# Performance work log

Measured on AMD Instinct MI355X. Metric: run time of the kernel, lower is better.

## Reference

```python
import jax, jax.numpy as jnp
import numpy as np

HIDDEN = 1024
HEADS = 16
HEAD_D = HIDDEN // HEADS
B = 64
MAX_S = 2048
EPS = 1e-5


def _layernorm(x, gamma, beta):
    mu = jnp.mean(x, axis=-1, keepdims=True)
    var = jnp.mean(jnp.square(x - mu), axis=-1, keepdims=True)
    return (x - mu) * jax.lax.rsqrt(var + EPS) * gamma + beta


def setup_inputs() -> dict:
    key = jax.random.key(0)
    ks = jax.random.split(key, 12)
    s = 1.0 / np.sqrt(HIDDEN)
    return {
        "seq": jax.random.normal(ks[0], (B, 1, HIDDEN), jnp.float32),
        "candidate_aa": jax.random.normal(ks[1], (B, 1, HIDDEN), jnp.float32),
        "k_cache": jax.random.normal(ks[2], (B, MAX_S, HEADS, HEAD_D), jnp.float32),
        "v_cache": jax.random.normal(ks[3], (B, MAX_S, HEADS, HEAD_D), jnp.float32),
        "cache_seqlens": jax.random.randint(ks[4], (B,), 0, MAX_S - 1, jnp.int32),
        "Wqkv": jax.random.normal(ks[5], (HIDDEN, 3 * HIDDEN), jnp.float32) * s,
        "bqkv": jnp.zeros((3 * HIDDEN,), jnp.float32),
        "Wc": jax.random.normal(ks[6], (HIDDEN, HIDDEN), jnp.float32) * s,
        "bc": jnp.zeros((HIDDEN,), jnp.float32),
        "Wo": jax.random.normal(ks[7], (HIDDEN, HIDDEN), jnp.float32) * s,
        "bo": jnp.zeros((HIDDEN,), jnp.float32),
        "gamma": jnp.ones((HIDDEN,), jnp.float32),
        "beta": jnp.zeros((HIDDEN,), jnp.float32),
    }


def reference(seq, candidate_aa, k_cache, v_cache, cache_seqlens,
              Wqkv, bqkv, Wc, bc, Wo, bo, gamma, beta):
    b = seq.shape[0]
    # fused QKV projection: [B,1,3*hidden] -> [B,1,H,3*D] -> chunk
    qkv = (seq @ Wqkv + bqkv).reshape(b, 1, HEADS, 3 * HEAD_D)
    q, k, v = jnp.split(qkv, 3, axis=-1)  # each [B,1,H,D]
    cand = candidate_aa @ Wc + bc
    # L2-normalize new k along head dim, then fp16 cast (as original)
    k = k / jnp.linalg.norm(k, axis=-1, keepdims=True)
    k = k.astype(jnp.float16).astype(k_cache.dtype)
    # write new token into caches at position cache_seqlens[b]
    bidx = jnp.arange(b)
    kc = k_cache.at[bidx, cache_seqlens].set(k[:, 0])
    vc = v_cache.at[bidx, cache_seqlens].set(v[:, 0])
    # attention over cache[:, :seqlen+1], softmax_scale = 1
    scores = jnp.einsum("bhd,bshd->bhs", q[:, 0], kc)  # [B,H,S]
    valid = jnp.arange(MAX_S)[None, None, :] <= cache_seqlens[:, None, None]
    scores = jnp.where(valid, scores, jnp.finfo(scores.dtype).min)
    p = jax.nn.softmax(scores, axis=-1)
    attn = jnp.einsum("bhs,bshd->bhd", p, vc).reshape(b, 1, HIDDEN)
    postx = attn @ Wo + bo
    candidate_out = _layernorm(postx + cand, gamma, beta)
    seq_out = _layernorm(seq + postx, gamma, beta)
    return (seq_out, candidate_out)
```

## Files before the change

### kernel.cpp

```cpp
#include <hip/hip_runtime.h>
#include <hip/hip_fp16.h>
#include <math.h>

#define HID   1024
#define NHEAD 16
#define HD    64
#define NB    64
#define MAXS  2048
#define CHUNK 256
#define NCH   (MAXS / CHUNK)
#define PS    68

typedef float f4v __attribute__((ext_vector_type(4)));
__device__ __forceinline__ float4 ntload4(const float* p) {
    f4v v = __builtin_nontemporal_load((const f4v*)p);
    return make_float4(v.x, v.y, v.z, v.w);
}

__global__ __launch_bounds__(1024) void proj_kernel(
    const float* __restrict__ seq, const float* __restrict__ cand,
    const float* __restrict__ Wqkv, const float* __restrict__ bqkv,
    const float* __restrict__ Wc,   const float* __restrict__ bcv,
    float* __restrict__ out )
{
    const int tid  = threadIdx.x;
    const int wv   = __builtin_amdgcn_readfirstlane(tid >> 6);
    const int lane = tid & 63;
    const int c0   = blockIdx.x * 16;
    const bool is_qkv = (c0 < 3072);
    const float* __restrict__ src  = is_qkv ? seq  : cand;
    const float* __restrict__ W    = is_qkv ? Wqkv : Wc;
    const float* __restrict__ bias = is_qkv ? bqkv : bcv;
    const int ldw = is_qkv ? 3072 : 1024;
    const int cb  = is_qkv ? c0 : (c0 - 3072);
    const int k0  = wv * 64;

    float acc[16];
    #pragma unroll
    for (int j = 0; j < 16; ++j) acc[j] = 0.f;

    const float4* sp = (const float4*)(src + lane * HID + k0);
    for (int kc = 0; kc < 16; ++kc) {
        float4 s4 = sp[kc];
        const float* wb = W + (size_t)(k0 + kc * 4) * ldw + cb;
        #pragma unroll
        for (int t = 0; t < 4; ++t) {
            float sv = (t == 0) ? s4.x : (t == 1) ? s4.y : (t == 2) ? s4.z : s4.w;
            const float4* wr = (const float4*)(wb + (size_t)t * ldw);
            #pragma unroll
            for (int j = 0; j < 4; ++j) {
                float4 w4 = wr[j];
                acc[4*j+0] = fmaf(sv, w4.x, acc[4*j+0]);
                acc[4*j+1] = fmaf(sv, w4.y, acc[4*j+1]);
                acc[4*j+2] = fmaf(sv, w4.z, acc[4*j+2]);
                acc[4*j+3] = fmaf(sv, w4.w, acc[4*j+3]);
            }
        }
    }

    __shared__ float red[16][16][64];
    #pragma unroll
    for (int j = 0; j < 16; ++j) red[wv][j][lane] = acc[j];
    __syncthreads();

    {
        const int j = tid >> 6, b = tid & 63;
        float s = 0.f;
        #pragma unroll
        for (int w = 0; w < 16; ++w) s += red[w][j][b];
        out[(c0 + j) * 64 + b] = s + bias[cb + j];
    }
}

__global__ __launch_bounds__(256) void attn_part_kernel(
    const float* __restrict__ proj, const float* __restrict__ k_cache,
    const float* __restrict__ v_cache, const int* __restrict__ seqlens,
    float* __restrict__ part)
{
    const int idx = blockIdx.x;
    const int c  = idx >> 10;
    const int bh = idx & 1023;
    const int b  = bh >> 4;
    const int h  = bh & 15;
    const int L  = seqlens[b];
    const int s0 = c << 8;
    if (s0 > L) return;

    const int tid = threadIdx.x;
    const int grp = tid >> 4;
    const int gl  = tid & 15;
    const bool has_new = (L < s0 + CHUNK);

    __shared__ float lq[64], lk[64], lv[64];
    __shared__ float sm_m[16], sm_l[16];
    __shared__ float sm_o[16][64];

    if (tid < 64) {
        lq[tid] = proj[(h * 192 + tid) * 64 + b];
    } else if (tid < 128) {
        if (has_new) {
            int d = tid - 64;
            float kr = proj[(h * 192 + 64 + d) * 64 + b];
            float ss = kr * kr;
            #pragma unroll
            for (int m = 1; m < 64; m <<= 1) ss += __shfl_xor(ss, m);
            float kn = kr / sqrtf(ss);
            lk[d] = __half2float(__float2half_rn(kn));
        }
    } else if (tid < 192) {
        if (has_new) {
            int d = tid - 128;
            lv[d] = proj[(h * 192 + 128 + d) * 64 + b];
        }
    }
    __syncthreads();

    const float4 q4 = ((const float4*)lq)[gl];
    const size_t base0 = (((size_t)b * MAXS) * NHEAD + h) * HD;

    float sc[16];
    float m, l;
    float4 o = make_float4(0.f, 0.f, 0.f, 0.f);

    if (!has_new) {
        #pragma unroll
        for (int t = 0; t < 16; ++t) {
            const int s = s0 + grp + t * 16;
            float4 k4 = ntload4(k_cache + base0 + (size_t)s * (NHEAD * HD) + gl * 4);
            float d = fmaf(k4.x, q4.x, fmaf(k4.y, q4.y, fmaf(k4.z, q4.z, k4.w * q4.w)));
            d += __shfl_xor(d, 1); d += __shfl_xor(d, 2);
            d += __shfl_xor(d, 4); d += __shfl_xor(d, 8);
            sc[t] = d;
        }
        m = sc[0];
        #pragma unroll
        for (int t = 1; t < 16; ++t) m = fmaxf(m, sc[t]);
        l = 0.f;
        #pragma unroll
        for (int t = 0; t < 16; ++t) { float p = __expf(sc[t] - m); sc[t] = p; l += p; }
        #pragma unroll
        for (int t = 0; t < 16; ++t) {
            const int s = s0 + grp + t * 16;
            float4 v4 = ntload4(v_cache + base0 + (size_t)s * (NHEAD * HD) + gl * 4);
            o.x = fmaf(sc[t], v4.x, o.x);
            o.y = fmaf(sc[t], v4.y, o.y);
            o.z = fmaf(sc[t], v4.z, o.z);
            o.w = fmaf(sc[t], v4.w, o.w);
        }
    } else {
        #pragma unroll
        for (int t = 0; t < 16; ++t) {
            const int s = s0 + grp + t * 16;
            float4 k4 = make_float4(0.f, 0.f, 0.f, 0.f);
            if (s < L)       k4 = ntload4(k_cache + base0 + (size_t)s * (NHEAD * HD) + gl * 4);
            else if (s == L) k4 = ((const float4*)lk)[gl];
            float d = fmaf(k4.x, q4.x, fmaf(k4.y, q4.y, fmaf(k4.z, q4.z, k4.w * q4.w)));
            d += __shfl_xor(d, 1); d += __shfl_xor(d, 2);
            d += __shfl_xor(d, 4); d += __shfl_xor(d, 8);
            sc[t] = (s <= L) ? d : -INFINITY;
        }
        m = sc[0];
        #pragma unroll
        for (int t = 1; t < 16; ++t) m = fmaxf(m, sc[t]);
        const float mm = (m == -INFINITY) ? 0.f : m;
        l = 0.f;
        #pragma unroll
        for (int t = 0; t < 16; ++t) { float p = __expf(sc[t] - mm); sc[t] = p; l += p; }
        #pragma unroll
        for (int t = 0; t < 16; ++t) {
            const int s = s0 + grp + t * 16;
            float4 v4 = make_float4(0.f, 0.f, 0.f, 0.f);
            if (s < L)       v4 = ntload4(v_cache + base0 + (size_t)s * (NHEAD * HD) + gl * 4);
            else if (s == L) v4 = ((const float4*)lv)[gl];
            o.x = fmaf(sc[t], v4.x, o.x);
            o.y = fmaf(sc[t], v4.y, o.y);
            o.z = fmaf(sc[t], v4.z, o.z);
            o.w = fmaf(sc[t], v4.w, o.w);
        }
    }

    if (gl == 0) { sm_m[grp] = m; sm_l[grp] = l; }
    ((float4*)sm_o[grp])[gl] = o;
    __syncthreads();

    if (tid < 64) {
        float M = -INFINITY;
        #pragma unroll
        for (int g = 0; g < 16; ++g) M = fmaxf(M, sm_m[g]);
        float li = 0.f, oi = 0.f;
        #pragma unroll
        for (int g = 0; g < 16; ++g) {
            float w = __expf(sm_m[g] - M);
            li += w * sm_l[g];
            oi += w * sm_o[g][tid];
        }
        float* pb = part + (size_t)(c * 1024 + bh) * PS;
        pb[tid] = oi;
        if (tid == 0) { pb[64] = M; pb[65] = li; }
    }
}

__global__ __launch_bounds__(64) void attn_merge_kernel(
    const float* __restrict__ part, const int* __restrict__ seqlens,
    float* __restrict__ attn_out )
{
    const int bh = blockIdx.x;
    const int b  = bh >> 4;
    const int h  = bh & 15;
    const int d  = threadIdx.x;
    const int nch = (seqlens[b] >> 8) + 1;

    float M = -INFINITY, l = 0.f, o = 0.f;
    for (int c = 0; c < nch; ++c) {
        const float* pb = part + (size_t)(c * 1024 + bh) * PS;
        float mc = pb[64], lc = pb[65];
        float Mn = fmaxf(M, mc);
        float f = __expf(M - Mn);
        float w = __expf(mc - Mn);
        o = o * f + w * pb[d];
        l = l * f + w * lc;
        M = Mn;
    }
    attn_out[(h * 64 + d) * 64 + b] = o / l;
}

__global__ __launch_bounds__(1024) void wo_kernel(
    const float* __restrict__ attn_s, const float* __restrict__ Wo,
    const float* __restrict__ bo, float* __restrict__ postx )
{
    const int tid  = threadIdx.x;
    const int wv   = __builtin_amdgcn_readfirstlane(tid >> 6);
    const int lane = tid & 63;
    const int c0   = blockIdx.x * 8;
    const int k0   = wv * 64;

    float acc[8];
    #pragma unroll
    for (int j = 0; j < 8; ++j) acc[j] = 0.f;

    for (int k = 0; k < 64; ++k) {
        float sv = attn_s[(k0 + k) * 64 + lane];
        const float4* wr = (const float4*)(Wo + (size_t)(k0 + k) * 1024 + c0);
        float4 w0 = wr[0], w1 = wr[1];
        acc[0] = fmaf(sv, w0.x, acc[0]); acc[1] = fmaf(sv, w0.y, acc[1]);
        acc[2] = fmaf(sv, w0.z, acc[2]); acc[3] = fmaf(sv, w0.w, acc[3]);
        acc[4] = fmaf(sv, w1.x, acc[4]); acc[5] = fmaf(sv, w1.y, acc[5]);
        acc[6] = fmaf(sv, w1.z, acc[6]); acc[7] = fmaf(sv, w1.w, acc[7]);
    }

    __shared__ float red[16][8][64];
    #pragma unroll
    for (int j = 0; j < 8; ++j) red[wv][j][lane] = acc[j];
    __syncthreads();

    if (tid < 512) {
        const int j = tid >> 6, b = tid & 63;
        float s = 0.f;
        #pragma unroll
        for (int w = 0; w < 16; ++w) s += red[w][j][b];
        postx[(c0 + j) * 64 + b] = s + bo[c0 + j];
    }
}

__global__ __launch_bounds__(256) void ln_kernel(
    const float* __restrict__ seq, const float* __restrict__ cand_s,
    const float* __restrict__ postx, const float* __restrict__ gamma,
    const float* __restrict__ beta, float* __restrict__ out)
{
    const int b   = blockIdx.x;
    const int tid = threadIdx.x;
    float x1[4], x2[4];
    float s1 = 0.f, q1 = 0.f, s2 = 0.f, q2 = 0.f;

    #pragma unroll
    for (int i = 0; i < 4; ++i) {
        int c = tid + i * 256;
        float px = postx[c * 64 + b];
        float sv = seq[b * HID + c];
        float cd = cand_s[c * 64 + b];
        float a = sv + px, d = px + cd;
        x1[i] = a; x2[i] = d;
        s1 += a; q1 += a * a; s2 += d; q2 += d * d;
    }
    #pragma unroll
    for (int m = 1; m < 64; m <<= 1) {
        s1 += __shfl_xor(s1, m); q1 += __shfl_xor(q1, m);
        s2 += __shfl_xor(s2, m); q2 += __shfl_xor(q2, m);
    }
    __shared__ float rsm[4][4];
    const int wv = tid >> 6, lane = tid & 63;
    if (lane == 0) { rsm[wv][0] = s1; rsm[wv][1] = q1; rsm[wv][2] = s2; rsm[wv][3] = q2; }
    __syncthreads();

    float S1 = rsm[0][0] + rsm[1][0] + rsm[2][0] + rsm[3][0];
    float Q1 = rsm[0][1] + rsm[1][1] + rsm[2][1] + rsm[3][1];
    float S2 = rsm[0][2] + rsm[1][2] + rsm[2][2] + rsm[3][2];
    float Q2 = rsm[0][3] + rsm[1][3] + rsm[2][3] + rsm[3][3];

    const float inv = 1.f / 1024.f;
    float mu1 = S1 * inv, v1 = Q1 * inv - mu1 * mu1;
    float mu2 = S2 * inv, v2 = Q2 * inv - mu2 * mu2;
    float r1 = rsqrtf(v1 + 1e-5f);
    float r2 = rsqrtf(v2 + 1e-5f);

    #pragma unroll
    for (int i = 0; i < 4; ++i) {
        int c = tid + i * 256;
        float g = gamma[c], be = beta[c];
        out[b * HID + c]            = (x1[i] - mu1) * r1 * g + be;
        out[NB * HID + b * HID + c] = (x2[i] - mu2) * r2 * g + be;
    }
}

extern "C" void kernel_launch(void* const* d_in, const int* in_sizes, int n_in,
                              void* d_out, int out_size, void* d_ws, size_t ws_size,
                              hipStream_t stream) {
    const float* seq      = (const float*)d_in[0];
    const float* cand     = (const float*)d_in[1];
    const float* k_cache  = (const float*)d_in[2];
    const float* v_cache  = (const float*)d_in[3];
    const int*   seqlens  = (const int*)  d_in[4];
    const float* Wqkv     = (const float*)d_in[5];
    const float* bqkv     = (const float*)d_in[6];
    const float* Wc       = (const float*)d_in[7];
    const float* bcv      = (const float*)d_in[8];
    const float* Wo       = (const float*)d_in[9];
    const float* bo       = (const float*)d_in[10];
    const float* gamma    = (const float*)d_in[11];
    const float* beta     = (const float*)d_in[12];
    float* out = (float*)d_out;

    float* ws    = (float*)d_ws;
    float* proj  = ws;
    float* attn  = proj  + 4096 * 64;
    float* postx = attn  + 1024 * 64;
    float* part  = postx + 1024 * 64;

    proj_kernel      <<<256, 1024, 0, stream>>>(seq, cand, Wqkv, bqkv, Wc, bcv, proj);
    attn_part_kernel <<<NCH * 1024, 256, 0, stream>>>(proj, k_cache, v_cache, seqlens, part);
    attn_merge_kernel<<<NB * NHEAD, 64, 0, stream>>>(part, seqlens, attn);
    wo_kernel        <<<128, 1024, 0, stream>>>(attn, Wo, bo, postx);
    ln_kernel        <<<NB, 256, 0, stream>>>(seq, proj + 3072 * 64, postx, gamma, beta, out);
}
```

Baseline: 149.5 us.

## Fuse attention merge, Wo projection and layernorms into one per-batch kernel

Replaces the merge, Wo GEMV and layernorm kernels with a single kernel that runs one 1024-thread block per batch row. Each block merges the chunk partials into a shared-memory attention row, multiplies it by the full Wo matrix, and applies both layernorms. This removes two launches and the global round trips for attn and postx. In exchange each of the 64 blocks streams all of Wo (4 MB) separately instead of the GEMV sharing weight loads across the batch, and only 64 blocks occupy the GPU.

```diff
diff --git a/kernel.cpp b/kernel.cpp
--- a/kernel.cpp
+++ b/kernel.cpp
@@ -200,116 +200,88 @@
     }
 }
 
-__global__ __launch_bounds__(64) void attn_merge_kernel(
-    const float* __restrict__ part, const int* __restrict__ seqlens,
-    float* __restrict__ attn_out )
-{
-    const int bh = blockIdx.x;
-    const int b  = bh >> 4;
-    const int h  = bh & 15;
-    const int d  = threadIdx.x;
-    const int nch = (seqlens[b] >> 8) + 1;
-
-    float M = -INFINITY, l = 0.f, o = 0.f;
-    for (int c = 0; c < nch; ++c) {
-        const float* pb = part + (size_t)(c * 1024 + bh) * PS;
-        float mc = pb[64], lc = pb[65];
-        float Mn = fmaxf(M, mc);
-        float f = __expf(M - Mn);
-        float w = __expf(mc - Mn);
-        o = o * f + w * pb[d];
-        l = l * f + w * lc;
-        M = Mn;
-    }
-    attn_out[(h * 64 + d) * 64 + b] = o / l;
-}
-
-__global__ __launch_bounds__(1024) void wo_kernel(
-    const float* __restrict__ attn_s, const float* __restrict__ Wo,
-    const float* __restrict__ bo, float* __restrict__ postx )
-{
-    const int tid  = threadIdx.x;
-    const int wv   = __builtin_amdgcn_readfirstlane(tid >> 6);
-    const int lane = tid & 63;
-    const int c0   = blockIdx.x * 8;
-    const int k0   = wv * 64;
-
-    float acc[8];
-    #pragma unroll
-    for (int j = 0; j < 8; ++j) acc[j] = 0.f;
-
-    for (int k = 0; k < 64; ++k) {
-        float sv = attn_s[(k0 + k) * 64 + lane];
-        const float4* wr = (const float4*)(Wo + (size_t)(k0 + k) * 1024 + c0);
-        float4 w0 = wr[0], w1 = wr[1];
-        acc[0] = fmaf(sv, w0.x, acc[0]); acc[1] = fmaf(sv, w0.y, acc[1]);
-        acc[2] = fmaf(sv, w0.z, acc[2]); acc[3] = fmaf(sv, w0.w, acc[3]);
-        acc[4] = fmaf(sv, w1.x, acc[4]); acc[5] = fmaf(sv, w1.y, acc[5]);
-        acc[6] = fmaf(sv, w1.z, acc[6]); acc[7] = fmaf(sv, w1.w, acc[7]);
-    }
-
-    __shared__ float red[16][8][64];
-    #pragma unroll
-    for (int j = 0; j < 8; ++j) red[wv][j][lane] = acc[j];
-    __syncthreads();
-
-    if (tid < 512) {
-        const int j = tid >> 6, b = tid & 63;
-        float s = 0.f;
-        #pragma unroll
-        for (int w = 0; w < 16; ++w) s += red[w][j][b];
-        postx[(c0 + j) * 64 + b] = s + bo[c0 + j];
-    }
-}
-
-__global__ __launch_bounds__(256) void ln_kernel(
-    const float* __restrict__ seq, const float* __restrict__ cand_s,
-    const float* __restrict__ postx, const float* __restrict__ gamma,
-    const float* __restrict__ beta, float* __restrict__ out)
+__global__ __launch_bounds__(1024) void post_kernel(
+    const float* __restrict__ proj, const float* __restrict__ part,
+    const int* __restrict__ seqlens, const float* __restrict__ Wo,
+    const float* __restrict__ bo, const float* __restrict__ seq,
+    const float* __restrict__ gamma, const float* __restrict__ beta,
+    float* __restrict__ out)
 {
     const int b   = blockIdx.x;
     const int tid = threadIdx.x;
-    float x1[4], x2[4];
-    float s1 = 0.f, q1 = 0.f, s2 = 0.f, q2 = 0.f;
-
-    #pragma unroll
-    for (int i = 0; i < 4; ++i) {
-        int c = tid + i * 256;
-        float px = postx[c * 64 + b];
-        float sv = seq[b * HID + c];
-        float cd = cand_s[c * 64 + b];
-        float a = sv + px, d = px + cd;
-        x1[i] = a; x2[i] = d;
-        s1 += a; q1 += a * a; s2 += d; q2 += d * d;
-    }
+    const int nch = (seqlens[b] >> 8) + 1;
+
+    __shared__ float attn_row[1024];
+    __shared__ float red[4][4][256];
+    __shared__ float rsm[16][4];
+
+    {
+        const int h = tid >> 6, d = tid & 63;
+        float M = -INFINITY, l = 0.f, o = 0.f;
+        for (int c = 0; c < nch; ++c) {
+            const float* pb = part + (size_t)(c * 1024 + b * 16 + h) * PS;
+            float mc = pb[64], lc = pb[65];
+            float Mn = fmaxf(M, mc);
+            float f = __expf(M - Mn);
+            float w = __expf(mc - Mn);
+            o = o * f + w * pb[d];
+            l = l * f + w * lc;
+            M = Mn;
+        }
+        attn_row[h * 64 + d] = o / l;
+    }
+    __syncthreads();
+
+    {
+        const int cg = tid & 255;
+        const int ks = tid >> 8;
+        float4 a = make_float4(0.f, 0.f, 0.f, 0.f);
+        const float* wp = Wo + (size_t)(ks * 256) * 1024 + cg * 4;
+        #pragma unroll 4
+        for (int k = 0; k < 256; ++k) {
+            float av = attn_row[ks * 256 + k];
+            float4 w4 = *(const float4*)(wp + (size_t)k * 1024);
+            a.x = fmaf(av, w4.x, a.x);
+            a.y = fmaf(av, w4.y, a.y);
+            a.z = fmaf(av, w4.z, a.z);
+            a.w = fmaf(av, w4.w, a.w);
+        }
+        red[ks][0][cg] = a.x; red[ks][1][cg] = a.y;
+        red[ks][2][cg] = a.z; red[ks][3][cg] = a.w;
+    }
+    __syncthreads();
+
+    const int c = tid;
+    float px = red[0][c & 3][c >> 2] + red[1][c & 3][c >> 2]
+             + red[2][c & 3][c >> 2] + red[3][c & 3][c >> 2] + bo[c];
+    float sv = seq[b * HID + c];
+    float cd = proj[(3072 + c) * 64 + b];
+    float x1 = sv + px, x2 = px + cd;
+
+    float s1 = x1, q1 = x1 * x1, s2 = x2, q2 = x2 * x2;
     #pragma unroll
     for (int m = 1; m < 64; m <<= 1) {
         s1 += __shfl_xor(s1, m); q1 += __shfl_xor(q1, m);
         s2 += __shfl_xor(s2, m); q2 += __shfl_xor(q2, m);
     }
-    __shared__ float rsm[4][4];
     const int wv = tid >> 6, lane = tid & 63;
     if (lane == 0) { rsm[wv][0] = s1; rsm[wv][1] = q1; rsm[wv][2] = s2; rsm[wv][3] = q2; }
     __syncthreads();
 
-    float S1 = rsm[0][0] + rsm[1][0] + rsm[2][0] + rsm[3][0];
-    float Q1 = rsm[0][1] + rsm[1][1] + rsm[2][1] + rsm[3][1];
-    float S2 = rsm[0][2] + rsm[1][2] + rsm[2][2] + rsm[3][2];
-    float Q2 = rsm[0][3] + rsm[1][3] + rsm[2][3] + rsm[3][3];
-
+    float S1 = 0.f, Q1 = 0.f, S2 = 0.f, Q2 = 0.f;
+    #pragma unroll
+    for (int w = 0; w < 16; ++w) {
+        S1 += rsm[w][0]; Q1 += rsm[w][1]; S2 += rsm[w][2]; Q2 += rsm[w][3];
+    }
     const float inv = 1.f / 1024.f;
     float mu1 = S1 * inv, v1 = Q1 * inv - mu1 * mu1;
     float mu2 = S2 * inv, v2 = Q2 * inv - mu2 * mu2;
     float r1 = rsqrtf(v1 + 1e-5f);
     float r2 = rsqrtf(v2 + 1e-5f);
 
-    #pragma unroll
-    for (int i = 0; i < 4; ++i) {
-        int c = tid + i * 256;
-        float g = gamma[c], be = beta[c];
-        out[b * HID + c]            = (x1[i] - mu1) * r1 * g + be;
-        out[NB * HID + b * HID + c] = (x2[i] - mu2) * r2 * g + be;
-    }
+    float g = gamma[c], be = beta[c];
+    out[b * HID + c]            = (x1 - mu1) * r1 * g + be;
+    out[NB * HID + b * HID + c] = (x2 - mu2) * r2 * g + be;
 }
 
 extern "C" void kernel_launch(void* const* d_in, const int* in_sizes, int n_in,
@@ -332,13 +304,9 @@
 
     float* ws    = (float*)d_ws;
     float* proj  = ws;
-    float* attn  = proj  + 4096 * 64;
-    float* postx = attn  + 1024 * 64;
-    float* part  = postx + 1024 * 64;
-
-    proj_kernel      <<<256, 1024, 0, stream>>>(seq, cand, Wqkv, bqkv, Wc, bcv, proj);
-    attn_part_kernel <<<NCH * 1024, 256, 0, stream>>>(proj, k_cache, v_cache, seqlens, part);
-    attn_merge_kernel<<<NB * NHEAD, 64, 0, stream>>>(part, seqlens, attn);
-    wo_kernel        <<<128, 1024, 0, stream>>>(attn, Wo, bo, postx);
-    ln_kernel        <<<NB, 256, 0, stream>>>(seq, proj + 3072 * 64, postx, gamma, beta, out);
-}
+    float* part  = proj + 4096 * 64;
+
+    proj_kernel     <<<256, 1024, 0, stream>>>(seq, cand, Wqkv, bqkv, Wc, bcv, proj);
+    attn_part_kernel<<<NCH * 1024, 256, 0, stream>>>(proj, k_cache, v_cache, seqlens, part);
+    post_kernel     <<<NB, 1024, 0, stream>>>(proj, part, seqlens, Wo, bo, seq, gamma, beta, out);
+}
```

New measurement: 165.4 us. +10.6%, slower.

## Split QKV/cand projection into split-K partial GEMV plus reduction kernel

Applied to the files above, without the earlier changes.

Replaces the single projection kernel with a split-K scheme. Each lane owns one output column and accumulates all 64 batch rows, reading each weight element once with nontemporal loads while the activations are broadcast from cache. A second kernel sums the 16 K-slice partials, adds the bias and writes a row-major projection buffer, and the attention and layernorm kernels now read that layout. This adds a kernel launch and a partial-sum buffer in global memory of about 16 MB written and read back, in exchange for better weight-stream efficiency.

```diff
diff --git a/kernel.cpp b/kernel.cpp
--- a/kernel.cpp
+++ b/kernel.cpp
@@ -10,70 +10,78 @@
 #define CHUNK 256
 #define NCH   (MAXS / CHUNK)
 #define PS    68
+#define NKS   16
 
 typedef float f4v __attribute__((ext_vector_type(4)));
 __device__ __forceinline__ float4 ntload4(const float* p) {
     f4v v = __builtin_nontemporal_load((const f4v*)p);
     return make_float4(v.x, v.y, v.z, v.w);
 }
-
-__global__ __launch_bounds__(1024) void proj_kernel(
+__device__ __forceinline__ float ntloadf(const float* p) {
+    return __builtin_nontemporal_load(p);
+}
+
+__global__ __launch_bounds__(256) void proj1_kernel(
     const float* __restrict__ seq, const float* __restrict__ cand,
-    const float* __restrict__ Wqkv, const float* __restrict__ bqkv,
-    const float* __restrict__ Wc,   const float* __restrict__ bcv,
-    float* __restrict__ out )
+    const float* __restrict__ Wqkv, const float* __restrict__ Wc,
+    float* __restrict__ partial )
 {
     const int tid  = threadIdx.x;
-    const int wv   = __builtin_amdgcn_readfirstlane(tid >> 6);
+    const int wv   = tid >> 6;
     const int lane = tid & 63;
-    const int c0   = blockIdx.x * 16;
-    const bool is_qkv = (c0 < 3072);
-    const float* __restrict__ src  = is_qkv ? seq  : cand;
-    const float* __restrict__ W    = is_qkv ? Wqkv : Wc;
-    const float* __restrict__ bias = is_qkv ? bqkv : bcv;
+    const int bid  = blockIdx.x;
+    const int cg   = bid & 63;
+    const int ks   = (bid >> 6) * 4 + wv;
+    const int k0   = ks * 64;
+    const bool is_qkv = (cg < 48);
+    const float* __restrict__ src = is_qkv ? seq  : cand;
+    const float* __restrict__ W   = is_qkv ? Wqkv : Wc;
     const int ldw = is_qkv ? 3072 : 1024;
-    const int cb  = is_qkv ? c0 : (c0 - 3072);
-    const int k0  = wv * 64;
-
-    float acc[16];
-    #pragma unroll
-    for (int j = 0; j < 16; ++j) acc[j] = 0.f;
-
-    const float4* sp = (const float4*)(src + lane * HID + k0);
-    for (int kc = 0; kc < 16; ++kc) {
-        float4 s4 = sp[kc];
-        const float* wb = W + (size_t)(k0 + kc * 4) * ldw + cb;
-        #pragma unroll
-        for (int t = 0; t < 4; ++t) {
-            float sv = (t == 0) ? s4.x : (t == 1) ? s4.y : (t == 2) ? s4.z : s4.w;
-            const float4* wr = (const float4*)(wb + (size_t)t * ldw);
-            #pragma unroll
-            for (int j = 0; j < 4; ++j) {
-                float4 w4 = wr[j];
-                acc[4*j+0] = fmaf(sv, w4.x, acc[4*j+0]);
-                acc[4*j+1] = fmaf(sv, w4.y, acc[4*j+1]);
-                acc[4*j+2] = fmaf(sv, w4.z, acc[4*j+2]);
-                acc[4*j+3] = fmaf(sv, w4.w, acc[4*j+3]);
-            }
-        }
-    }
-
-    __shared__ float red[16][16][64];
-    #pragma unroll
-    for (int j = 0; j < 16; ++j) red[wv][j][lane] = acc[j];
-    __syncthreads();
-
-    {
-        const int j = tid >> 6, b = tid & 63;
-        float s = 0.f;
-        #pragma unroll
-        for (int w = 0; w < 16; ++w) s += red[w][j][b];
-        out[(c0 + j) * 64 + b] = s + bias[cb + j];
-    }
+    const int col = is_qkv ? (cg * 64 + lane) : ((cg - 48) * 64 + lane);
+    const int gcol = cg * 64 + lane;
+
+    float acc[64];
+    #pragma unroll
+    for (int b = 0; b < 64; ++b) acc[b] = 0.f;
+
+    const float* wp = W + (size_t)k0 * ldw + col;
+    const float* sp = src + k0;
+
+    for (int kq = 0; kq < 16; ++kq) {
+        const float* wq = wp + (size_t)(kq * 4) * ldw;
+        float w0 = ntloadf(wq);
+        float w1 = ntloadf(wq + ldw);
+        float w2 = ntloadf(wq + 2 * (size_t)ldw);
+        float w3 = ntloadf(wq + 3 * (size_t)ldw);
+        #pragma unroll
+        for (int b = 0; b < 64; ++b) {
+            float4 s4 = *(const float4*)(sp + b * HID + kq * 4);
+            acc[b] = fmaf(s4.x, w0, fmaf(s4.y, w1,
+                     fmaf(s4.z, w2, fmaf(s4.w, w3, acc[b]))));
+        }
+    }
+
+    float* pb = partial + (size_t)(ks * 64) * 4096 + gcol;
+    #pragma unroll
+    for (int b = 0; b < 64; ++b) pb[(size_t)b * 4096] = acc[b];
+}
+
+__global__ __launch_bounds__(1024) void proj2_kernel(
+    const float* __restrict__ partial, const float* __restrict__ bqkv,
+    const float* __restrict__ bcv, float* __restrict__ projRM )
+{
+    const int T   = blockIdx.x * 1024 + threadIdx.x;
+    const int b   = T >> 12;
+    const int col = T & 4095;
+    float v = (col < 3072) ? bqkv[col] : bcv[col - 3072];
+    #pragma unroll
+    for (int ks = 0; ks < NKS; ++ks)
+        v += partial[(size_t)(ks * 64 + b) * 4096 + col];
+    projRM[(size_t)b * 4096 + col] = v;
 }
 
 __global__ __launch_bounds__(256) void attn_part_kernel(
-    const float* __restrict__ proj, const float* __restrict__ k_cache,
+    const float* __restrict__ projRM, const float* __restrict__ k_cache,
     const float* __restrict__ v_cache, const int* __restrict__ seqlens,
     float* __restrict__ part)
 {
@@ -90,17 +98,18 @@
     const int grp = tid >> 4;
     const int gl  = tid & 15;
     const bool has_new = (L < s0 + CHUNK);
+    const float* prow = projRM + (size_t)b * 4096 + h * 192;
 
     __shared__ float lq[64], lk[64], lv[64];
     __shared__ float sm_m[16], sm_l[16];
     __shared__ float sm_o[16][64];
 
     if (tid < 64) {
-        lq[tid] = proj[(h * 192 + tid) * 64 + b];
+        lq[tid] = prow[tid];
     } else if (tid < 128) {
         if (has_new) {
             int d = tid - 64;
-            float kr = proj[(h * 192 + 64 + d) * 64 + b];
+            float kr = prow[64 + d];
             float ss = kr * kr;
             #pragma unroll
             for (int m = 1; m < 64; m <<= 1) ss += __shfl_xor(ss, m);
@@ -110,7 +119,7 @@
     } else if (tid < 192) {
         if (has_new) {
             int d = tid - 128;
-            lv[d] = proj[(h * 192 + 128 + d) * 64 + b];
+            lv[d] = prow[128 + d];
         }
     }
     __syncthreads();
@@ -263,7 +272,7 @@
 }
 
 __global__ __launch_bounds__(256) void ln_kernel(
-    const float* __restrict__ seq, const float* __restrict__ cand_s,
+    const float* __restrict__ seq, const float* __restrict__ projRM,
     const float* __restrict__ postx, const float* __restrict__ gamma,
     const float* __restrict__ beta, float* __restrict__ out)
 {
@@ -277,7 +286,7 @@
         int c = tid + i * 256;
         float px = postx[c * 64 + b];
         float sv = seq[b * HID + c];
-        float cd = cand_s[c * 64 + b];
+        float cd = projRM[(size_t)b * 4096 + 3072 + c];
         float a = sv + px, d = px + cd;
         x1[i] = a; x2[i] = d;
         s1 += a; q1 += a * a; s2 += d; q2 += d * d;
@@ -330,15 +339,17 @@
     const float* beta     = (const float*)d_in[12];
     float* out = (float*)d_out;
 
-    float* ws    = (float*)d_ws;
-    float* proj  = ws;
-    float* attn  = proj  + 4096 * 64;
-    float* postx = attn  + 1024 * 64;
-    float* part  = postx + 1024 * 64;
-
-    proj_kernel      <<<256, 1024, 0, stream>>>(seq, cand, Wqkv, bqkv, Wc, bcv, proj);
-    attn_part_kernel <<<NCH * 1024, 256, 0, stream>>>(proj, k_cache, v_cache, seqlens, part);
+    float* ws      = (float*)d_ws;
+    float* projRM  = ws;
+    float* attn    = projRM + 64 * 4096;
+    float* postx   = attn   + 1024 * 64;
+    float* part    = postx  + 1024 * 64;
+    float* partial = part   + NCH * 1024 * PS;
+
+    proj1_kernel     <<<256, 256, 0, stream>>>(seq, cand, Wqkv, Wc, partial);
+    proj2_kernel     <<<256, 1024, 0, stream>>>(partial, bqkv, bcv, projRM);
+    attn_part_kernel <<<NCH * 1024, 256, 0, stream>>>(projRM, k_cache, v_cache, seqlens, part);
     attn_merge_kernel<<<NB * NHEAD, 64, 0, stream>>>(part, seqlens, attn);
     wo_kernel        <<<128, 1024, 0, stream>>>(attn, Wo, bo, postx);
-    ln_kernel        <<<NB, 256, 0, stream>>>(seq, proj + 3072 * 64, postx, gamma, beta, out);
-}
+    ln_kernel        <<<NB, 256, 0, stream>>>(seq, projRM, postx, gamma, beta, out);
+}
```

Result: slower. 203.5 us (+36.2%).
